# Optimization experiments

Measured on AMD Instinct MI355X. Metric: run time of the kernel, lower is better.

The kernel has to match this reference:

```python
import jax, jax.numpy as jnp
import numpy as np

D_MODEL = 2048
N_HEADS = 16
D_K = D_MODEL // N_HEADS
D_FF = ((int(D_MODEL * 8 / 3) + 63) // 64) * 64  # 5504
B, S = 2, 2048
EPS = 1e-6


def setup_inputs() -> dict:
    key = jax.random.key(0)
    ks = jax.random.split(key, 16)
    sc = 0.02
    x = jax.random.normal(ks[0], (B, S, D_MODEL), dtype=jnp.float32)
    mask = jnp.tril(jnp.ones((S, S), dtype=jnp.int32))[None]  # [1,S,S] causal
    inp = {
        'x': x,
        'mask': mask,
        'wq': jax.random.normal(ks[1], (D_MODEL, D_MODEL), jnp.float32) * sc,
        'bq': jnp.zeros((D_MODEL,), jnp.float32),
        'wk': jax.random.normal(ks[2], (D_MODEL, D_MODEL), jnp.float32) * sc,
        'bk': jnp.zeros((D_MODEL,), jnp.float32),
        'wv': jax.random.normal(ks[3], (D_MODEL, D_MODEL), jnp.float32) * sc,
        'bv': jnp.zeros((D_MODEL,), jnp.float32),
        'wo': jax.random.normal(ks[4], (D_MODEL, D_MODEL), jnp.float32) * sc,
        'bo': jnp.zeros((D_MODEL,), jnp.float32),
        'g1': jnp.ones((D_MODEL,), jnp.float32),  # RMSNorm weights
        'g2': jnp.ones((D_MODEL,), jnp.float32),
        'w1': jax.random.normal(ks[5], (D_MODEL, D_FF), jnp.float32) * sc,
        'w3': jax.random.normal(ks[6], (D_MODEL, D_FF), jnp.float32) * sc,
        'w2': jax.random.normal(ks[7], (D_FF, D_MODEL), jnp.float32) * sc,
    }
    return inp


def _rmsnorm(x, w):
    rms = jnp.sqrt(jnp.mean(x * x, axis=-1, keepdims=True) + EPS)
    return x / rms * w


def _block(x, mask, wq, bq, wk, bk, wv, bv, wo, bo, g1, g2, w1, w2, w3):
    b, s, _ = x.shape
    # --- attention sublayer (pre-LN) ---
    n = _rmsnorm(x, g1)
    q = (n @ wq + bq).reshape(b, s, N_HEADS, D_K).transpose(0, 2, 1, 3)
    k = (n @ wk + bk).reshape(b, s, N_HEADS, D_K).transpose(0, 2, 1, 3)
    v = (n @ wv + bv).reshape(b, s, N_HEADS, D_K).transpose(0, 2, 1, 3)
    scores = jnp.einsum('bhqd,bhkd->bhqk', q, k) / jnp.sqrt(jnp.float32(D_K))
    m = mask[:, None, :, :]  # [1,1,S,S]
    scores = jnp.where(m == 0, jnp.float32(-jnp.inf), scores)
    attn = jax.nn.softmax(scores, axis=-1)
    ao = jnp.einsum('bhqk,bhkd->bhqd', attn, v)
    ao = ao.transpose(0, 2, 1, 3).reshape(b, s, D_MODEL)
    x = x + (ao @ wo + bo)
    # --- SwiGLU FFN sublayer (pre-LN) ---
    n = _rmsnorm(x, g2)
    ffn = (jax.nn.silu(n @ w1) * (n @ w3)) @ w2
    return x + ffn


def reference(x, mask, wq, bq, wk, bk, wv, bv, wo, bo, g1, g2, w1, w2, w3):
    return _block(x, mask, wq, bq, wk, bk, wv, bv, wo, bo, g1, g2, w1, w2, w3)
```

## Files before the change

kernel.cpp:

```cpp
#include <hip/hip_runtime.h>
#include <stdint.h>

typedef unsigned short u16;
typedef __bf16 bf16x8 __attribute__((ext_vector_type(8)));
typedef float f32x4 __attribute__((ext_vector_type(4)));

#define D_MODEL 2048
#define NHEADS 16
#define DK 128
#define DFF 5504
#define DFFP 5632
#define BB 2
#define SS 2048
#define MTOK 4096
#define DQKV 6144

#define AS1 __attribute__((address_space(1)))
#define AS3 __attribute__((address_space(3)))

__device__ __forceinline__ u16 f2bf(float f){
  union { float f; uint32_t u; } v; v.f = f;
  uint32_t r = v.u + 0x7fffu + ((v.u >> 16) & 1u);
  return (u16)(r >> 16);
}
__device__ __forceinline__ float bf2f(u16 u){
  union { uint32_t u; float f; } v; v.u = ((uint32_t)u) << 16;
  return v.f;
}
__device__ __forceinline__ u16 cvt_bf16(float f){
  union { __bf16 h; u16 u; } v; v.h = (__bf16)f; return v.u;
}
__device__ __forceinline__ float fexp2(float x){
#if __has_builtin(__builtin_amdgcn_exp2f)
  return __builtin_amdgcn_exp2f(x);
#else
  return exp2f(x);
#endif
}

__global__ __launch_bounds__(256) void k_transpose_w(const float* __restrict__ W,
                                                     u16* __restrict__ Wt, int K, int Nsrc){
  __shared__ float tile[32][33];
  int n0 = blockIdx.x * 32, k0 = blockIdx.y * 32;
  int tx = threadIdx.x, ty = threadIdx.y;
  #pragma unroll
  for (int r = 0; r < 4; ++r){
    int n = n0 + tx;
    tile[ty + r*8][tx] = (n < Nsrc) ? W[(size_t)(k0 + ty + r*8) * Nsrc + n] : 0.0f;
  }
  __syncthreads();
  #pragma unroll
  for (int r = 0; r < 4; ++r)
    Wt[(size_t)(n0 + ty + r*8) * K + k0 + tx] = f2bf(tile[tx][ty + r*8]);
}

__global__ __launch_bounds__(256) void k_transpose_v(const u16* __restrict__ V,
                                                     u16* __restrict__ Vt, int ld){
  __shared__ u16 tile[32][33];
  int s0 = blockIdx.x * 32;
  int bh = blockIdx.y >> 2, dt = blockIdx.y & 3;
  int b = bh >> 4, h = bh & 15;
  int tx = threadIdx.x, ty = threadIdx.y;
  #pragma unroll
  for (int r = 0; r < 4; ++r)
    tile[ty + r*8][tx] = V[(size_t)(b*SS + s0 + ty + r*8) * ld + h*DK + dt*32 + tx];
  __syncthreads();
  #pragma unroll
  for (int r = 0; r < 4; ++r)
    Vt[(size_t)(bh*DK + dt*32 + ty + r*8) * SS + s0 + tx] = tile[tx][ty + r*8];
}

__global__ __launch_bounds__(256) void k_concat3(const float* __restrict__ a,
                                                 const float* __restrict__ b,
                                                 const float* __restrict__ c,
                                                 float* __restrict__ o){
  int i = blockIdx.x*256 + threadIdx.x;
  if (i >= DQKV) return;
  o[i] = (i < 2048) ? a[i] : (i < 4096 ? b[i-2048] : c[i-4096]);
}

__global__ __launch_bounds__(256) void k_rmsnorm(const float* __restrict__ X,
                                                 const float* __restrict__ g,
                                                 u16* __restrict__ out){
  int row = blockIdx.x, tid = threadIdx.x;
  const float* x = X + (size_t)row * D_MODEL;
  float4 a = ((const float4*)x)[tid*2];
  float4 b = ((const float4*)x)[tid*2+1];
  float ss = a.x*a.x + a.y*a.y + a.z*a.z + a.w*a.w
           + b.x*b.x + b.y*b.y + b.z*b.z + b.w*b.w;
  #pragma unroll
  for (int m = 1; m < 64; m <<= 1) ss += __shfl_xor(ss, m, 64);
  __shared__ float red[4];
  if ((tid & 63) == 0) red[tid >> 6] = ss;
  __syncthreads();
  float tot = red[0] + red[1] + red[2] + red[3];
  float sc = rsqrtf(tot * (1.0f / D_MODEL) + 1e-6f);
  float4 ga = ((const float4*)g)[tid*2];
  float4 gb = ((const float4*)g)[tid*2+1];
  uint32_t w0 = f2bf(a.x*sc*ga.x) | ((uint32_t)f2bf(a.y*sc*ga.y) << 16);
  uint32_t w1 = f2bf(a.z*sc*ga.z) | ((uint32_t)f2bf(a.w*sc*ga.w) << 16);
  uint32_t w2 = f2bf(b.x*sc*gb.x) | ((uint32_t)f2bf(b.y*sc*gb.y) << 16);
  uint32_t w3 = f2bf(b.z*sc*gb.z) | ((uint32_t)f2bf(b.w*sc*gb.w) << 16);
  ((uint4*)(out + (size_t)row * D_MODEL))[tid] = make_uint4(w0, w1, w2, w3);
}

template<int EPI>
__global__ __launch_bounds__(512, 2) void k_gemm8p(
    const u16* __restrict__ A, const u16* __restrict__ Bt,
    const float* __restrict__ bias, const u16* __restrict__ aux,
    void* __restrict__ Cout, int M, int N, int K,
    int lda, int ldb, int ldc)
{
  extern __shared__ __align__(16) char smem[];
  const int tid = threadIdx.x;
  const int lane = tid & 63, wid = tid >> 6;
  const int wr = wid >> 2, wc = wid & 3;
  const int lrow = lane & 15, lhi = lane >> 4;

  int nwg = gridDim.x, wg = blockIdx.x;
  int qq = nwg >> 3, rr = nwg & 7;
  int xcd = wg & 7, sub = wg >> 3;
  int swz = (xcd < rr ? xcd*(qq+1) : rr*(qq+1) + (xcd-rr)*qq) + sub;
  int nbx = N >> 8;
  int m0 = (swz / nbx) << 8, n0 = (swz % nbx) << 8;

  const int nk = K >> 6;
  const int hA = wr, hB = wc >> 1;
  const int gA = wc;
  const int gB = (wr << 1) | (wc & 1);

  auto stA = [&](int d, int kk, int q){
    #pragma unroll
    for (int L = 0; L < 2; ++L){
      int p = q*8192 + gA*2048 + L*1024 + lane*16;
      int row = p >> 7;
      int o = (p & 127) ^ ((row & 7) << 4);
      __builtin_amdgcn_global_load_lds(
        (const AS1 void*)(A + (size_t)(m0 + hA*128 + row)*lda + kk + (o >> 1)),
        (AS3 void*)(smem + d*65536 + hA*16384 + p), 16, 0, 0);
    }
  };
  auto stB = [&](int d, int kk, int s){
    #pragma unroll
    for (int L = 0; L < 2; ++L){
      int p = s*4096 + (gB >> 1)*8192 + (gB & 1)*2048 + L*1024 + lane*16;
      int row = p >> 7;
      int o = (p & 127) ^ ((row & 7) << 4);
      __builtin_amdgcn_global_load_lds(
        (const AS1 void*)(Bt + (size_t)(n0 + hB*128 + row)*ldb + kk + (o >> 1)),
        (AS3 void*)(smem + d*65536 + 32768 + hB*16384 + p), 16, 0, 0);
    }
  };
  auto rdA = [&](int d, int rloc, int ks)->bf16x8{
    int p = rloc*128 + ((ks*64 + lhi*16) ^ ((rloc & 7) << 4));
    return *(const bf16x8*)(smem + d*65536 + hA*16384 + p);
  };
  auto rdB = [&](int d, int rloc, int ks)->bf16x8{
    int p = rloc*128 + ((ks*64 + lhi*16) ^ ((rloc & 7) << 4));
    return *(const bf16x8*)(smem + d*65536 + 32768 + hB*16384 + p);
  };

  f32x4 acc[8][4] = {};

  stA(0, 0, 0); stB(0, 0, 0); stB(0, 0, 1); stA(0, 0, 1);
  asm volatile("s_waitcnt vmcnt(0)" ::: "memory");
  __builtin_amdgcn_s_barrier();

  for (int t = 0; t < nk; ++t){
    int d = t & 1, dn = d ^ 1, kkn = (t + 1) << 6;
    bool pf = (t + 1 < nk);
    bf16x8 aR[8], bQ0[4], bQ1[4];

    #pragma unroll
    for (int ii = 0; ii < 4; ++ii){
      aR[ii*2]   = rdA(d, ii*16 + lrow, 0);
      aR[ii*2+1] = rdA(d, ii*16 + lrow, 1);
    }
    #pragma unroll
    for (int j = 0; j < 2; ++j){
      bQ0[j*2]   = rdB(d, (wc&1)*64 + j*16 + lrow, 0);
      bQ0[j*2+1] = rdB(d, (wc&1)*64 + j*16 + lrow, 1);
    }
    if (pf){ stA(dn, kkn, 0); stB(dn, kkn, 0); }
    asm volatile("s_waitcnt lgkmcnt(0)" ::: "memory");
    __builtin_amdgcn_sched_barrier(0);
    __builtin_amdgcn_s_setprio(1);
    #pragma unroll
    for (int ii = 0; ii < 4; ++ii)
      #pragma unroll
      for (int j = 0; j < 2; ++j){
        acc[ii][j] = __builtin_amdgcn_mfma_f32_16x16x32_bf16(aR[ii*2],   bQ0[j*2],   acc[ii][j], 0, 0, 0);
        acc[ii][j] = __builtin_amdgcn_mfma_f32_16x16x32_bf16(aR[ii*2+1], bQ0[j*2+1], acc[ii][j], 0, 0, 0);
      }
    __builtin_amdgcn_s_setprio(0);
    if (pf) asm volatile("s_waitcnt vmcnt(6)" ::: "memory");
    else    asm volatile("s_waitcnt vmcnt(2)" ::: "memory");
    __builtin_amdgcn_sched_barrier(0);
    __builtin_amdgcn_s_barrier();

    #pragma unroll
    for (int j = 0; j < 2; ++j){
      bQ1[j*2]   = rdB(d, (wc&1)*64 + 32 + j*16 + lrow, 0);
      bQ1[j*2+1] = rdB(d, (wc&1)*64 + 32 + j*16 + lrow, 1);
    }
    if (pf) stB(dn, kkn, 1);
    asm volatile("s_waitcnt lgkmcnt(0)" ::: "memory");
    __builtin_amdgcn_sched_barrier(0);
    __builtin_amdgcn_s_setprio(1);
    #pragma unroll
    for (int ii = 0; ii < 4; ++ii)
      #pragma unroll
      for (int j = 0; j < 2; ++j){
        acc[ii][2+j] = __builtin_amdgcn_mfma_f32_16x16x32_bf16(aR[ii*2],   bQ1[j*2],   acc[ii][2+j], 0, 0, 0);
        acc[ii][2+j] = __builtin_amdgcn_mfma_f32_16x16x32_bf16(aR[ii*2+1], bQ1[j*2+1], acc[ii][2+j], 0, 0, 0);
      }
    __builtin_amdgcn_s_setprio(0);
    if (pf) asm volatile("s_waitcnt vmcnt(6)" ::: "memory");
    else    asm volatile("s_waitcnt vmcnt(0)" ::: "memory");
    __builtin_amdgcn_sched_barrier(0);
    __builtin_amdgcn_s_barrier();

    #pragma unroll
    for (int ii = 0; ii < 4; ++ii){
      aR[ii*2]   = rdA(d, 64 + ii*16 + lrow, 0);
      aR[ii*2+1] = rdA(d, 64 + ii*16 + lrow, 1);
    }
    if (pf) stA(dn, kkn, 1);
    asm volatile("s_waitcnt lgkmcnt(0)" ::: "memory");
    __builtin_amdgcn_sched_barrier(0);
    __builtin_amdgcn_s_setprio(1);
    #pragma unroll
    for (int ii = 0; ii < 4; ++ii)
      #pragma unroll
      for (int j = 0; j < 2; ++j){
        acc[4+ii][2+j] = __builtin_amdgcn_mfma_f32_16x16x32_bf16(aR[ii*2],   bQ1[j*2],   acc[4+ii][2+j], 0, 0, 0);
        acc[4+ii][2+j] = __builtin_amdgcn_mfma_f32_16x16x32_bf16(aR[ii*2+1], bQ1[j*2+1], acc[4+ii][2+j], 0, 0, 0);
      }
    __builtin_amdgcn_s_setprio(0);
    __builtin_amdgcn_s_barrier();

    __builtin_amdgcn_s_setprio(1);
    #pragma unroll
    for (int ii = 0; ii < 4; ++ii)
      #pragma unroll
      for (int j = 0; j < 2; ++j){
        acc[4+ii][j] = __builtin_amdgcn_mfma_f32_16x16x32_bf16(aR[ii*2],   bQ0[j*2],   acc[4+ii][j], 0, 0, 0);
        acc[4+ii][j] = __builtin_amdgcn_mfma_f32_16x16x32_bf16(aR[ii*2+1], bQ0[j*2+1], acc[4+ii][j], 0, 0, 0);
      }
    __builtin_amdgcn_s_setprio(0);
    if (pf) asm volatile("s_waitcnt vmcnt(4)" ::: "memory");
    __builtin_amdgcn_sched_barrier(0);
    __builtin_amdgcn_s_barrier();
  }

  #pragma unroll
  for (int i = 0; i < 8; ++i){
    #pragma unroll
    for (int j = 0; j < 4; ++j){
      int col = n0 + wc*64 + j*16 + lrow;
      float bv = 0.f;
      if constexpr (EPI == 0) bv = bias[col];
      #pragma unroll
      for (int q = 0; q < 4; ++q){
        int row = m0 + wr*128 + i*16 + lhi*4 + q;
        size_t idx = (size_t)row*ldc + col;
        float v = acc[i][j][q] + bv;
        if constexpr (EPI == 4){
          float a0v = bf2f(aux[idx]);
          v = a0v / (1.f + __expf(-a0v)) * v;
        }
        ((u16*)Cout)[idx] = f2bf(v);
      }
    }
  }
}

template<int EPI>
__global__ __launch_bounds__(256) void k_gemm_bt(
    const u16* __restrict__ A, const u16* __restrict__ Bt,
    const float* __restrict__ bias, const float* __restrict__ res,
    const u16* __restrict__ aux,
    void* __restrict__ Cout, int M, int N, int K,
    int lda, int ldb, int ldc)
{
  __shared__ __align__(16) u16 As[3][128*32];
  __shared__ __align__(16) u16 Bs[3][128*32];
  int tid = threadIdx.x;

  int nwg = gridDim.x, wg = blockIdx.x;
  int qq = nwg >> 3, rr = nwg & 7;
  int xcd = wg & 7, sub = wg >> 3;
  int swz = (xcd < rr ? xcd*(qq+1) : rr*(qq+1) + (xcd-rr)*qq) + sub;
  int nbx = N >> 7;
  int m0 = (swz / nbx) << 7, n0 = (swz % nbx) << 7;

  int lane = tid & 63, wave = tid >> 6;
  int wr = wave >> 1, wc = wave & 1;
  int lrow = lane & 15, lhi = lane >> 4;
  f32x4 acc[4][4] = {};
  int srow = tid >> 2;
  int schk = tid & 3;
  const int nk = K >> 5;

  auto stage = [&](int slot, int kt){
    int k0 = kt << 5;
    int c = schk ^ (srow & 3);
    #pragma unroll
    for (int cc = 0; cc < 2; ++cc){
      int r = cc*64 + srow;
      __builtin_amdgcn_global_load_lds(
        (const AS1 void*)(A + (size_t)(m0 + r)*lda + k0 + c*8),
        (AS3 void*)(&As[slot][r*32 + schk*8]), 16, 0, 0);
      __builtin_amdgcn_global_load_lds(
        (const AS1 void*)(Bt + (size_t)(n0 + r)*ldb + k0 + c*8),
        (AS3 void*)(&Bs[slot][r*32 + schk*8]), 16, 0, 0);
    }
  };

  stage(0, 0);
  if (nk > 1) stage(1, 1);
  if (nk > 1) asm volatile("s_waitcnt vmcnt(4)" ::: "memory");
  else        asm volatile("s_waitcnt vmcnt(0)" ::: "memory");
  __builtin_amdgcn_s_barrier();

  for (int kt = 0; kt < nk; ++kt){
    int cur = kt % 3;
    if (kt + 2 < nk) stage((kt + 2) % 3, kt + 2);
    int rchk = lhi ^ (lrow & 3);
    bf16x8 af[4], bfv[4];
    #pragma unroll
    for (int i = 0; i < 4; ++i){
      af[i]  = *(const bf16x8*)(&As[cur][(wr*64 + i*16 + lrow)*32 + rchk*8]);
      bfv[i] = *(const bf16x8*)(&Bs[cur][(wc*64 + i*16 + lrow)*32 + rchk*8]);
    }
    #pragma unroll
    for (int i = 0; i < 4; ++i)
      #pragma unroll
      for (int j = 0; j < 4; ++j)
        acc[i][j] = __builtin_amdgcn_mfma_f32_16x16x32_bf16(af[i], bfv[j], acc[i][j], 0, 0, 0);
    if (kt + 2 < nk) asm volatile("s_waitcnt vmcnt(4)" ::: "memory");
    else             asm volatile("s_waitcnt vmcnt(0)" ::: "memory");
    __builtin_amdgcn_s_barrier();
  }

  #pragma unroll
  for (int i = 0; i < 4; ++i){
    #pragma unroll
    for (int j = 0; j < 4; ++j){
      int col = n0 + wc*64 + j*16 + lrow;
      float bv = 0.f;
      if constexpr (EPI == 0 || EPI == 1) bv = bias[col];
      #pragma unroll
      for (int q = 0; q < 4; ++q){
        int row = m0 + wr*64 + i*16 + lhi*4 + q;
        size_t idx = (size_t)row*ldc + col;
        float v = acc[i][j][q] + bv;
        if constexpr (EPI == 1 || EPI == 3) v += res[idx];
        if constexpr (EPI == 4){
          float a0 = bf2f(aux[idx]);
          v = a0 / (1.f + __expf(-a0)) * v;
        }
        if constexpr (EPI == 0 || EPI == 2 || EPI == 4) ((u16*)Cout)[idx] = f2bf(v);
        else ((float*)Cout)[idx] = v;
      }
    }
  }
}

__global__ __launch_bounds__(512) void k_attn(
    const u16* __restrict__ Q, const u16* __restrict__ Kb,
    const u16* __restrict__ Vt, u16* __restrict__ O, int ldq)
{
  int tid = threadIdx.x, lane = tid & 63, wave = tid >> 6;
  int lrow = lane & 15, lhi = lane >> 4;
  int bidx = blockIdx.x;
  int bh = bidx >> 3, j = bidx & 7;
  int b = bh >> 4, h = bh & 15;

  __shared__ __align__(16) u16 Kbuf[2][64*128];
  __shared__ __align__(16) u16 Vbuf[2][128*64];
  __shared__ __align__(16) u16 P_lds[8][16*64];
  char* pw = (char*)&P_lds[wave][0];
  const float sc2 = 0.08838834764831845f * 1.44269504088896340736f;

  auto stage = [&](int bufi, int kt){
    int kv0 = kt << 6;
    char* kd = (char*)&Kbuf[bufi][0];
    char* vd = (char*)&Vbuf[bufi][0];
    #pragma unroll
    for (int L = 0; L < 2; ++L){
      int cid = wave*128 + L*64 + lane;
      int r = cid >> 4, c = cid & 15;
      int cg = c ^ (r & 7);
      __builtin_amdgcn_global_load_lds(
        (const AS1 void*)(Kb + (size_t)(b*SS + kv0 + r)*ldq + h*DK + cg*8),
        (AS3 void*)(kd + wave*2048 + L*1024 + lane*16), 16, 0, 0);
      int dd = cid >> 3, c8 = cid & 7;
      int cv = c8 ^ (dd & 7);
      __builtin_amdgcn_global_load_lds(
        (const AS1 void*)(Vt + (size_t)bh*DK*SS + (size_t)dd*SS + kv0 + cv*8),
        (AS3 void*)(vd + wave*2048 + L*1024 + lane*16), 16, 0, 0);
    }
  };

  #pragma unroll 1
  for (int item = 0; item < 2; ++item){
    int qi = item == 0 ? 15 - j : j;
    int qs = qi * 128;
    int nt = 2*qi + 2;
    int qrow = qs + wave * 16;

    bf16x8 qf[4];
    const u16* qbase = Q + (size_t)(b*SS + qrow + lrow)*ldq + h*DK + lhi*8;
    #pragma unroll
    for (int dc = 0; dc < 4; ++dc) qf[dc] = *(const bf16x8*)(qbase + dc*32);

    f32x4 accO[8] = {};
    float mr[4] = {-1e30f,-1e30f,-1e30f,-1e30f};
    float lr[4] = {0.f,0.f,0.f,0.f};

    stage(0, 0);
    __syncthreads();

    for (int kt = 0; kt < nt; ++kt){
      int cur = kt & 1;
      if (kt + 1 < nt) stage(cur ^ 1, kt + 1);
      int kv0 = kt << 6;
      if (kv0 <= qrow + 15){
        const char* kl = (const char*)&Kbuf[cur][0];
        const char* vl = (const char*)&Vbuf[cur][0];
        bool domask = (kv0 + 63 > qrow);

        f32x4 sf[4];
        #pragma unroll
        for (int hf = 0; hf < 4; ++hf){
          int rl = hf*16 + lrow;
          int sw = rl & 7;
          f32x4 a = {};
          #pragma unroll
          for (int dc = 0; dc < 4; ++dc){
            bf16x8 kf = *(const bf16x8*)(kl + rl*256 + (((lhi + dc*4) ^ sw) << 4));
            a = __builtin_amdgcn_mfma_f32_16x16x32_bf16(qf[dc], kf, a, 0, 0, 0);
          }
          sf[hf] = a;
        }

        float p[4][4], mx[4];
        #pragma unroll
        for (int q = 0; q < 4; ++q){
          float s0 = sf[0][q]*sc2, s1 = sf[1][q]*sc2, s2 = sf[2][q]*sc2, s3 = sf[3][q]*sc2;
          if (domask){
            int qg = qrow + lhi*4 + q;
            if (kv0      + lrow > qg) s0 = -1e30f;
            if (kv0 + 16 + lrow > qg) s1 = -1e30f;
            if (kv0 + 32 + lrow > qg) s2 = -1e30f;
            if (kv0 + 48 + lrow > qg) s3 = -1e30f;
          }
          p[q][0]=s0; p[q][1]=s1; p[q][2]=s2; p[q][3]=s3;
          float m = fmaxf(fmaxf(s0,s1), fmaxf(s2,s3));
          m = fmaxf(m, __shfl_xor(m, 1, 64));
          m = fmaxf(m, __shfl_xor(m, 2, 64));
          m = fmaxf(m, __shfl_xor(m, 4, 64));
          m = fmaxf(m, __shfl_xor(m, 8, 64));
          mx[q] = m;
        }
        float dmax = fmaxf(fmaxf(mx[0]-mr[0], mx[1]-mr[1]), fmaxf(mx[2]-mr[2], mx[3]-mr[3]));
        bool rescale = !__all(dmax <= 8.0f);
        float al[4];
        #pragma unroll
        for (int q = 0; q < 4; ++q){
          if (rescale){
            float mn = fmaxf(mr[q], mx[q]);
            al[q] = fexp2(mr[q] - mn);
            mr[q] = mn;
          } else al[q] = 1.0f;
          p[q][0] = fexp2(p[q][0] - mr[q]);
          p[q][1] = fexp2(p[q][1] - mr[q]);
          p[q][2] = fexp2(p[q][2] - mr[q]);
          p[q][3] = fexp2(p[q][3] - mr[q]);
          float sm = (p[q][0] + p[q][1]) + (p[q][2] + p[q][3]);
          sm += __shfl_xor(sm, 1, 64);
          sm += __shfl_xor(sm, 2, 64);
          sm += __shfl_xor(sm, 4, 64);
          sm += __shfl_xor(sm, 8, 64);
          lr[q] = lr[q]*al[q] + sm;
        }
        if (rescale){
          #pragma unroll
          for (int f = 0; f < 8; ++f)
            #pragma unroll
            for (int q = 0; q < 4; ++q) accO[f][q] *= al[q];
        }

        #pragma unroll
        for (int q = 0; q < 4; ++q){
          int row = lhi*4 + q;
          int rb = row*128, sw = (row & 7) << 4;
          #pragma unroll
          for (int hf = 0; hf < 4; ++hf)
            *(u16*)(pw + rb + ((hf*32 + lrow*2) ^ sw)) = cvt_bf16(p[q][hf]);
        }
        __builtin_amdgcn_sched_barrier(0);
        int rsw = (lrow & 7) << 4;
        bf16x8 pa0 = *(const bf16x8*)(pw + lrow*128 + ((     lhi*16) ^ rsw));
        bf16x8 pa1 = *(const bf16x8*)(pw + lrow*128 + ((64 + lhi*16) ^ rsw));

        #pragma unroll
        for (int f = 0; f < 8; ++f){
          int d = f*16 + lrow;
          int swv = d & 7;
          bf16x8 v0 = *(const bf16x8*)(vl + d*128 + (((lhi    ) ^ swv) << 4));
          bf16x8 v1 = *(const bf16x8*)(vl + d*128 + (((lhi + 4) ^ swv) << 4));
          accO[f] = __builtin_amdgcn_mfma_f32_16x16x32_bf16(pa0, v0, accO[f], 0, 0, 0);
          accO[f] = __builtin_amdgcn_mfma_f32_16x16x32_bf16(pa1, v1, accO[f], 0, 0, 0);
        }
      }
      __syncthreads();
    }

    #pragma unroll
    for (int q = 0; q < 4; ++q){
      float inv = 1.0f / lr[q];
      #pragma unroll
      for (int f = 0; f < 8; ++f){
        int row = b*SS + qrow + lhi*4 + q;
        int col = h*DK + f*16 + lrow;
        O[(size_t)row*D_MODEL + col] = cvt_bf16(accO[f][q] * inv);
      }
    }
    __syncthreads();
  }
}

extern "C" void kernel_launch(void* const* d_in, const int* in_sizes, int n_in,
                              void* d_out, int out_size, void* d_ws, size_t ws_size,
                              hipStream_t stream)
{
  (void)in_sizes; (void)n_in; (void)out_size;
  const float* x  = (const float*)d_in[0];
  const float* wq = (const float*)d_in[2];
  const float* bq = (const float*)d_in[3];
  const float* wk = (const float*)d_in[4];
  const float* bk = (const float*)d_in[5];
  const float* wv = (const float*)d_in[6];
  const float* bv = (const float*)d_in[7];
  const float* wo = (const float*)d_in[8];
  const float* bo = (const float*)d_in[9];
  const float* g1 = (const float*)d_in[10];
  const float* g2 = (const float*)d_in[11];
  const float* w1 = (const float*)d_in[12];
  const float* w3 = (const float*)d_in[13];
  const float* w2 = (const float*)d_in[14];
  float* out = (float*)d_out;

  const size_t MB = 1u << 20;
  const size_t WFF2 = (size_t)D_MODEL * DFF * sizeof(u16);
  const size_t NEED = 112*MB + WFF2 + 32768;
  if (ws_size < NEED) return;
  char* ws = (char*)d_ws;
  u16* bufA = (u16*)(ws + 0);
  u16* qkv  = (u16*)(ws + 16*MB);
  u16* h1   = qkv;
  u16* wqkvt= (u16*)(ws + 64*MB);
  u16* w1t  = wqkvt;
  u16* wot  = (u16*)(ws + 88*MB);
  u16* w3t  = (u16*)(ws + 88*MB);
  u16* vtb  = (u16*)(ws + 96*MB);
  u16* w2t  = (u16*)(ws + 112*MB);
  float* bqkv = (float*)(ws + 112*MB + WFF2);

  bool big = true;
  big &= hipFuncSetAttribute((const void*)k_gemm8p<0>, hipFuncAttributeMaxDynamicSharedMemorySize, 131072) == hipSuccess;
  big &= hipFuncSetAttribute((const void*)k_gemm8p<2>, hipFuncAttributeMaxDynamicSharedMemorySize, 131072) == hipSuccess;
  big &= hipFuncSetAttribute((const void*)k_gemm8p<4>, hipFuncAttributeMaxDynamicSharedMemorySize, 131072) == hipSuccess;

  dim3 tb(32, 8);
  k_transpose_w<<<dim3(64,64), tb, 0, stream>>>(wq, wqkvt,               D_MODEL, D_MODEL);
  k_transpose_w<<<dim3(64,64), tb, 0, stream>>>(wk, wqkvt + 2048*2048,   D_MODEL, D_MODEL);
  k_transpose_w<<<dim3(64,64), tb, 0, stream>>>(wv, wqkvt + 2*2048*2048, D_MODEL, D_MODEL);
  k_transpose_w<<<dim3(64,64), tb, 0, stream>>>(wo, wot, D_MODEL, D_MODEL);
  k_transpose_w<<<dim3(64, DFF/32), tb, 0, stream>>>(w2, w2t, DFF, D_MODEL);
  k_concat3<<<24, 256, 0, stream>>>(bq, bk, bv, bqkv);

  k_rmsnorm<<<MTOK, 256, 0, stream>>>(x, g1, bufA);
  if (big)
    k_gemm8p<0><<<(MTOK/256)*(DQKV/256), 512, 131072, stream>>>(bufA, wqkvt, bqkv, nullptr, qkv, MTOK, DQKV, D_MODEL, D_MODEL, D_MODEL, DQKV);
  else
    k_gemm_bt<0><<<(DQKV/128)*(MTOK/128), 256, 0, stream>>>(bufA, wqkvt, bqkv, nullptr, nullptr, qkv, MTOK, DQKV, D_MODEL, D_MODEL, D_MODEL, DQKV);
  k_transpose_v<<<dim3(SS/32, 128), tb, 0, stream>>>(qkv + 4096, vtb, DQKV);
  k_attn<<<dim3(BB*NHEADS*8), 512, 0, stream>>>(qkv, qkv + 2048, vtb, bufA, DQKV);
  k_transpose_w<<<dim3(DFFP/32, 64), tb, 0, stream>>>(w1, w1t, D_MODEL, DFF);
  k_gemm_bt<1><<<16*32, 256, 0, stream>>>(bufA, wot, bo, x, nullptr, out, MTOK, D_MODEL, D_MODEL, D_MODEL, D_MODEL, D_MODEL);
  k_transpose_w<<<dim3(DFFP/32, 64), tb, 0, stream>>>(w3, w3t, D_MODEL, DFF);
  k_rmsnorm<<<MTOK, 256, 0, stream>>>(out, g2, bufA);
  if (big){
    k_gemm8p<2><<<(MTOK/256)*(DFFP/256), 512, 131072, stream>>>(bufA, w1t, nullptr, nullptr, h1, MTOK, DFFP, D_MODEL, D_MODEL, D_MODEL, DFFP);
    k_gemm8p<4><<<(MTOK/256)*(DFFP/256), 512, 131072, stream>>>(bufA, w3t, nullptr, h1, h1, MTOK, DFFP, D_MODEL, D_MODEL, D_MODEL, DFFP);
  } else {
    k_gemm_bt<2><<<(DFFP/128)*32, 256, 0, stream>>>(bufA, w1t, nullptr, nullptr, nullptr, h1, MTOK, DFFP, D_MODEL, D_MODEL, D_MODEL, DFFP);
    k_gemm_bt<4><<<(DFFP/128)*32, 256, 0, stream>>>(bufA, w3t, nullptr, nullptr, h1, h1, MTOK, DFFP, D_MODEL, D_MODEL, D_MODEL, DFFP);
  }
  k_gemm_bt<3><<<16*32, 256, 0, stream>>>(h1, w2t, nullptr, out, nullptr, out, MTOK, D_MODEL, DFF, DFFP, DFF, D_MODEL);
}
```

Before: 735.7 us.

## Merge W1/W3 GEMMs into one launch with XCD-aware tile mapping

The two separate FFN up-projection GEMMs become a single GEMM over concatenated transposed W1|W3 weights. The epilogue routes the second half of the columns into a separate h3 buffer, and a new elementwise SiLU-multiply kernel combines them. Blocks are now mapped to XCDs as 2x4 regions for better L2 locality, and extra workgroup barriers are added after issuing the prefetch in each pipeline phase. The aim is to share the A-operand reads and cut tail effects, at the cost of an extra full-size round trip for h3 and the added barriers.

```diff
diff --git a/kernel.cpp b/kernel.cpp
--- a/kernel.cpp
+++ b/kernel.cpp
@@ -104,6 +104,27 @@
   ((uint4*)(out + (size_t)row * D_MODEL))[tid] = make_uint4(w0, w1, w2, w3);
 }
 
+__global__ __launch_bounds__(256) void k_silu_mul(const u16* __restrict__ a,
+                                                  const u16* __restrict__ b,
+                                                  u16* __restrict__ o, int n8){
+  int i = blockIdx.x * 256 + threadIdx.x;
+  if (i >= n8) return;
+  uint4 av = ((const uint4*)a)[i];
+  uint4 bv = ((const uint4*)b)[i];
+  uint32_t aa[4] = {av.x, av.y, av.z, av.w};
+  uint32_t bb[4] = {bv.x, bv.y, bv.z, bv.w};
+  uint32_t rr[4];
+  #pragma unroll
+  for (int j = 0; j < 4; ++j){
+    float x0 = bf2f((u16)(aa[j] & 0xffff)), x1 = bf2f((u16)(aa[j] >> 16));
+    float y0 = bf2f((u16)(bb[j] & 0xffff)), y1 = bf2f((u16)(bb[j] >> 16));
+    float r0 = x0 / (1.f + __expf(-x0)) * y0;
+    float r1 = x1 / (1.f + __expf(-x1)) * y1;
+    rr[j] = f2bf(r0) | ((uint32_t)f2bf(r1) << 16);
+  }
+  ((uint4*)o)[i] = make_uint4(rr[0], rr[1], rr[2], rr[3]);
+}
+
 template<int EPI>
 __global__ __launch_bounds__(512, 2) void k_gemm8p(
     const u16* __restrict__ A, const u16* __restrict__ Bt,
@@ -118,11 +139,19 @@
   const int lrow = lane & 15, lhi = lane >> 4;
 
   int nwg = gridDim.x, wg = blockIdx.x;
-  int qq = nwg >> 3, rr = nwg & 7;
+  int nbx = N >> 8, nbm = M >> 8;
   int xcd = wg & 7, sub = wg >> 3;
-  int swz = (xcd < rr ? xcd*(qq+1) : rr*(qq+1) + (xcd-rr)*qq) + sub;
-  int nbx = N >> 8;
-  int m0 = (swz / nbx) << 8, n0 = (swz % nbx) << 8;
+  int m0, n0;
+  if ((nwg & 7) == 0 && (nbm & 1) == 0 && (nbx & 3) == 0){
+    int mh = nbm >> 1;
+    int mr = sub % mh, nc = sub / mh;
+    m0 = (((xcd & 1) * mh) + mr) << 8;
+    n0 = (((xcd >> 1) * (nbx >> 2)) + nc) << 8;
+  } else {
+    int qq = nwg >> 3, rr2 = nwg & 7;
+    int swz = (xcd < rr2 ? xcd*(qq+1) : rr2*(qq+1) + (xcd-rr2)*qq) + sub;
+    m0 = (swz / nbx) << 8; n0 = (swz % nbx) << 8;
+  }
 
   const int nk = K >> 6;
   const int hA = wr, hB = wc >> 1;
@@ -182,6 +211,7 @@
       bQ0[j*2+1] = rdB(d, (wc&1)*64 + j*16 + lrow, 1);
     }
     if (pf){ stA(dn, kkn, 0); stB(dn, kkn, 0); }
+    __builtin_amdgcn_s_barrier();
     asm volatile("s_waitcnt lgkmcnt(0)" ::: "memory");
     __builtin_amdgcn_sched_barrier(0);
     __builtin_amdgcn_s_setprio(1);
@@ -204,6 +234,7 @@
       bQ1[j*2+1] = rdB(d, (wc&1)*64 + 32 + j*16 + lrow, 1);
     }
     if (pf) stB(dn, kkn, 1);
+    __builtin_amdgcn_s_barrier();
     asm volatile("s_waitcnt lgkmcnt(0)" ::: "memory");
     __builtin_amdgcn_sched_barrier(0);
     __builtin_amdgcn_s_setprio(1);
@@ -226,6 +257,7 @@
       aR[ii*2+1] = rdA(d, 64 + ii*16 + lrow, 1);
     }
     if (pf) stA(dn, kkn, 1);
+    __builtin_amdgcn_s_barrier();
     asm volatile("s_waitcnt lgkmcnt(0)" ::: "memory");
     __builtin_amdgcn_sched_barrier(0);
     __builtin_amdgcn_s_setprio(1);
@@ -253,6 +285,11 @@
     __builtin_amdgcn_s_barrier();
   }
 
+  u16* Cw = (u16*)Cout;
+  int cofs = 0;
+  if constexpr (EPI == 5){
+    if (n0 >= 5632){ Cw = (u16*)aux; cofs = 5632; }
+  }
   #pragma unroll
   for (int i = 0; i < 8; ++i){
     #pragma unroll
@@ -263,13 +300,8 @@
       #pragma unroll
       for (int q = 0; q < 4; ++q){
         int row = m0 + wr*128 + i*16 + lhi*4 + q;
-        size_t idx = (size_t)row*ldc + col;
         float v = acc[i][j][q] + bv;
-        if constexpr (EPI == 4){
-          float a0v = bf2f(aux[idx]);
-          v = a0v / (1.f + __expf(-a0v)) * v;
-        }
-        ((u16*)Cout)[idx] = f2bf(v);
+        Cw[(size_t)row*ldc + (col - cofs)] = f2bf(v);
       }
     }
   }
@@ -554,25 +586,24 @@
   float* out = (float*)d_out;
 
   const size_t MB = 1u << 20;
-  const size_t WFF2 = (size_t)D_MODEL * DFF * sizeof(u16);
-  const size_t NEED = 112*MB + WFF2 + 32768;
+  const size_t W2T_B = (size_t)D_MODEL * DFF * sizeof(u16);
+  const size_t NEED = 152*MB + W2T_B + 32768;
   if (ws_size < NEED) return;
   char* ws = (char*)d_ws;
-  u16* bufA = (u16*)(ws + 0);
-  u16* qkv  = (u16*)(ws + 16*MB);
-  u16* h1   = qkv;
-  u16* wqkvt= (u16*)(ws + 64*MB);
-  u16* w1t  = wqkvt;
-  u16* wot  = (u16*)(ws + 88*MB);
-  u16* w3t  = (u16*)(ws + 88*MB);
-  u16* vtb  = (u16*)(ws + 96*MB);
-  u16* w2t  = (u16*)(ws + 112*MB);
-  float* bqkv = (float*)(ws + 112*MB + WFF2);
+  u16* bufA  = (u16*)(ws + 0);
+  u16* qkv   = (u16*)(ws + 16*MB);
+  u16* h1    = qkv;
+  u16* wqkvt = (u16*)(ws + 64*MB);
+  u16* w1w3t = (u16*)(ws + 64*MB);
+  u16* wot   = (u16*)(ws + 88*MB);
+  u16* vtb   = (u16*)(ws + 96*MB);
+  u16* h3    = (u16*)(ws + 108*MB);
+  u16* w2t   = (u16*)(ws + 152*MB);
+  float* bqkv = (float*)(ws + 152*MB + W2T_B);
 
   bool big = true;
   big &= hipFuncSetAttribute((const void*)k_gemm8p<0>, hipFuncAttributeMaxDynamicSharedMemorySize, 131072) == hipSuccess;
-  big &= hipFuncSetAttribute((const void*)k_gemm8p<2>, hipFuncAttributeMaxDynamicSharedMemorySize, 131072) == hipSuccess;
-  big &= hipFuncSetAttribute((const void*)k_gemm8p<4>, hipFuncAttributeMaxDynamicSharedMemorySize, 131072) == hipSuccess;
+  big &= hipFuncSetAttribute((const void*)k_gemm8p<5>, hipFuncAttributeMaxDynamicSharedMemorySize, 131072) == hipSuccess;
 
   dim3 tb(32, 8);
   k_transpose_w<<<dim3(64,64), tb, 0, stream>>>(wq, wqkvt,               D_MODEL, D_MODEL);
@@ -588,17 +619,17 @@
   else
     k_gemm_bt<0><<<(DQKV/128)*(MTOK/128), 256, 0, stream>>>(bufA, wqkvt, bqkv, nullptr, nullptr, qkv, MTOK, DQKV, D_MODEL, D_MODEL, D_MODEL, DQKV);
   k_transpose_v<<<dim3(SS/32, 128), tb, 0, stream>>>(qkv + 4096, vtb, DQKV);
+  k_transpose_w<<<dim3(DFFP/32, 64), tb, 0, stream>>>(w1, w1w3t, D_MODEL, DFF);
   k_attn<<<dim3(BB*NHEADS*8), 512, 0, stream>>>(qkv, qkv + 2048, vtb, bufA, DQKV);
-  k_transpose_w<<<dim3(DFFP/32, 64), tb, 0, stream>>>(w1, w1t, D_MODEL, DFF);
   k_gemm_bt<1><<<16*32, 256, 0, stream>>>(bufA, wot, bo, x, nullptr, out, MTOK, D_MODEL, D_MODEL, D_MODEL, D_MODEL, D_MODEL);
-  k_transpose_w<<<dim3(DFFP/32, 64), tb, 0, stream>>>(w3, w3t, D_MODEL, DFF);
+  k_transpose_w<<<dim3(DFFP/32, 64), tb, 0, stream>>>(w3, w1w3t + (size_t)DFFP*2048, D_MODEL, DFF);
   k_rmsnorm<<<MTOK, 256, 0, stream>>>(out, g2, bufA);
   if (big){
-    k_gemm8p<2><<<(MTOK/256)*(DFFP/256), 512, 131072, stream>>>(bufA, w1t, nullptr, nullptr, h1, MTOK, DFFP, D_MODEL, D_MODEL, D_MODEL, DFFP);
-    k_gemm8p<4><<<(MTOK/256)*(DFFP/256), 512, 131072, stream>>>(bufA, w3t, nullptr, h1, h1, MTOK, DFFP, D_MODEL, D_MODEL, D_MODEL, DFFP);
+    k_gemm8p<5><<<(MTOK/256)*((2*DFFP)/256), 512, 131072, stream>>>(bufA, w1w3t, nullptr, h3, h1, MTOK, 2*DFFP, D_MODEL, D_MODEL, D_MODEL, DFFP);
   } else {
-    k_gemm_bt<2><<<(DFFP/128)*32, 256, 0, stream>>>(bufA, w1t, nullptr, nullptr, nullptr, h1, MTOK, DFFP, D_MODEL, D_MODEL, D_MODEL, DFFP);
-    k_gemm_bt<4><<<(DFFP/128)*32, 256, 0, stream>>>(bufA, w3t, nullptr, nullptr, h1, h1, MTOK, DFFP, D_MODEL, D_MODEL, D_MODEL, DFFP);
-  }
+    k_gemm_bt<2><<<(DFFP/128)*32, 256, 0, stream>>>(bufA, w1w3t, nullptr, nullptr, nullptr, h1, MTOK, DFFP, D_MODEL, D_MODEL, D_MODEL, DFFP);
+    k_gemm_bt<2><<<(DFFP/128)*32, 256, 0, stream>>>(bufA, w1w3t + (size_t)DFFP*2048, nullptr, nullptr, nullptr, h3, MTOK, DFFP, D_MODEL, D_MODEL, D_MODEL, DFFP);
+  }
+  k_silu_mul<<<(MTOK*DFFP/8 + 255)/256, 256, 0, stream>>>(h1, h3, h1, MTOK*DFFP/8);
   k_gemm_bt<3><<<16*32, 256, 0, stream>>>(h1, w2t, nullptr, out, nullptr, out, MTOK, D_MODEL, DFF, DFFP, DFF, D_MODEL);
 }
```

Result: no change. 721.8 us (-1.9%).
